# Optimization experiments

Hardware: AMD Instinct MI355X
Metric: run time of the kernel (lower is better)

The kernel has to match this reference:

```python
import jax, jax.numpy as jnp
import numpy as np

SEQ, BATCH, D_IN, D_HID, D_OUT = 2048, 256, 512, 512, 1000


def setup_inputs() -> dict:
    key = jax.random.key(0)
    ks = jax.random.split(key, 15)
    s_in = 1.0 / np.sqrt(D_IN)
    s_h = 1.0 / np.sqrt(D_HID)
    def lin(k, fan_in, shape, scale):
        return jax.random.uniform(k, shape, jnp.float32, -scale, scale)
    return {
        "x": jax.random.normal(ks[0], (SEQ, BATCH, D_IN), jnp.float32),
        # weights stored as [in, out] so y = x @ W + b
        "Wz": lin(ks[1], D_IN, (D_IN, D_HID), s_in),  "bz": lin(ks[2], D_IN, (D_HID,), s_in),
        "Uz": lin(ks[3], D_HID, (D_HID, D_HID), s_h), "buz": lin(ks[4], D_HID, (D_HID,), s_h),
        "Wr": lin(ks[5], D_IN, (D_IN, D_HID), s_in),  "br": lin(ks[6], D_IN, (D_HID,), s_in),
        "Ur": lin(ks[7], D_HID, (D_HID, D_HID), s_h), "bur": lin(ks[8], D_HID, (D_HID,), s_h),
        "Wh": lin(ks[9], D_IN, (D_IN, D_HID), s_in),  "bh": lin(ks[10], D_IN, (D_HID,), s_in),
        "Uh": lin(ks[11], D_HID, (D_HID, D_HID), s_h), "buh": lin(ks[12], D_HID, (D_HID,), s_h),
        "Wfc": lin(ks[13], D_HID, (D_HID, D_OUT), s_h), "bfc": lin(ks[14], D_HID, (D_OUT,), s_h),
    }


def reference(x, Wz, bz, Uz, buz, Wr, br, Ur, bur, Wh, bh, Uh, buh, Wfc, bfc):
    B, H = x.shape[1], Uz.shape[0]

    def gru_step(h, xt):
        # xt: [B, D_IN], h: [B, H]
        z = jax.nn.sigmoid(xt @ Wz + bz + h @ Uz + buz)
        r = jax.nn.sigmoid(xt @ Wr + br + h @ Ur + bur)
        h_tild = jnp.tanh(xt @ Wh + bh + (r * h) @ Uh + buh)
        h_new = (1.0 - z) * h + z * h_tild
        return h_new, None

    h0 = jnp.zeros((B, H), x.dtype)  # zero init hidden (broadcast-equivalent)
    h, _ = jax.lax.scan(gru_step, h0, x)
    out = jax.nn.relu(h) @ Wfc + bfc        # [B, D_OUT]
    out = out[None]                          # [1, B, D_OUT]
    return jax.nn.log_softmax(out, axis=1)  # dim=1 as in torch module
```

## Files before the change

### kernel.cpp

```cpp
#include <hip/hip_runtime.h>


typedef unsigned short ushort_t;
typedef unsigned int uint_t;
typedef __bf16 bf16_t;
typedef bf16_t bf16x8 __attribute__((ext_vector_type(8)));
typedef float f32x4 __attribute__((ext_vector_type(4)));
typedef uint_t u32x4 __attribute__((ext_vector_type(4)));

__device__ __forceinline__ ushort_t f2bf(float f) {
  uint_t u = __float_as_uint(f);
  u += 0x7FFFu + ((u >> 16) & 1u);
  return (ushort_t)(u >> 16);
}
__device__ __forceinline__ float bfu2f(uint_t h) { return __uint_as_float(h << 16); }

__device__ __forceinline__ uint_t atom_add_ret(uint_t* p, uint_t v) {
  uint_t old;
  asm volatile("global_atomic_add %0, %1, %2, off sc0\n\t"
               "s_waitcnt vmcnt(0)"
               : "=v"(old) : "v"(p), "v"(v) : "memory");
  return old;
}
__device__ __forceinline__ void atom_add_noret(uint_t* p, uint_t v) {
  asm volatile("global_atomic_add %0, %1, off" :: "v"(p), "v"(v) : "memory");
}

__global__ __launch_bounds__(256) void prep_kernel(
    const float* __restrict__ Wz, const float* __restrict__ Wr, const float* __restrict__ Wh,
    const float* __restrict__ Uz, const float* __restrict__ Ur, const float* __restrict__ Uh,
    const float* __restrict__ bz, const float* __restrict__ buz,
    const float* __restrict__ br, const float* __restrict__ bur,
    const float* __restrict__ bh, const float* __restrict__ buh,
    ushort_t* __restrict__ UT, ushort_t* __restrict__ WT, float* __restrict__ gbias)
{
  const int idx = blockIdx.x * 256 + threadIdx.x;
  {
    const int gate = idx >> 18, n = (idx >> 9) & 511, k = idx & 511;
    const float* U = (gate == 0) ? Uz : (gate == 1 ? Ur : Uh);
    UT[idx] = f2bf(U[k * 512 + n]);
  }
  {
    const int n = idx >> 9, k = idx & 511;
    const int gate = n >> 9, nn = n & 511;
    const float* W = (gate == 0) ? Wz : (gate == 1 ? Wr : Wh);
    WT[idx] = f2bf(W[k * 512 + nn]);
  }
  if (idx < 1536) {
    const int gate = idx >> 9, nn = idx & 511;
    gbias[idx] = (gate == 0) ? (bz[nn] + buz[nn])
               : (gate == 1) ? (br[nn] + bur[nn])
                             : (bh[nn] + buh[nn]);
  }
}

__global__ __launch_bounds__(256) void gate_gemm(
    const float* __restrict__ x,
    const ushort_t* __restrict__ WT,
    const float* __restrict__ gbias,
    ushort_t* __restrict__ gout,
    int mtiles)
{
  __shared__ ushort_t A_sh[128 * 72];
  __shared__ ushort_t B_sh[128 * 72];
  const int bid = blockIdx.x;
  int mt, nt;
  if ((mtiles & 31) == 0) {
    const int sb = bid / 384;
    const int r = bid - sb * 384;
    mt = sb * 32 + (r & 31);
    nt = r >> 5;
  } else {
    mt = bid / 12;
    nt = bid - mt * 12;
  }
  const int mrow0 = mt * 128;
  const int ncol0 = nt * 128;
  const int tid = threadIdx.x;
  const int wid = tid >> 6;
  const int lane = tid & 63;
  const int wm = wid >> 1, wn = wid & 1;
  const int l15 = lane & 15, l4 = lane >> 4;

  const f32x4 vzero = {0.f, 0.f, 0.f, 0.f};
  f32x4 acc[4][4];
#pragma unroll
  for (int m = 0; m < 4; ++m)
#pragma unroll
    for (int n = 0; n < 4; ++n) acc[m][n] = vzero;

  const int ar = tid >> 4, ak = tid & 15;
  const int bn = tid >> 3, bk = tid & 7;

  for (int ks = 0; ks < 8; ++ks) {
    if (ks) __syncthreads();
    const int k0 = ks * 64;
#pragma unroll
    for (int p = 0; p < 8; ++p) {
      const int r = p * 16 + ar;
      const float4 v = *(const float4*)&x[(size_t)(mrow0 + r) * 512 + (k0 + ak * 4)];
      ushort4 hv;
      hv.x = f2bf(v.x); hv.y = f2bf(v.y); hv.z = f2bf(v.z); hv.w = f2bf(v.w);
      *(ushort4*)&A_sh[r * 72 + ak * 4] = hv;
    }
#pragma unroll
    for (int p = 0; p < 4; ++p) {
      const int n = p * 32 + bn;
      *(uint4*)&B_sh[n * 72 + bk * 8] =
          *(const uint4*)&WT[(size_t)(ncol0 + n) * 512 + (k0 + bk * 8)];
    }
    __syncthreads();
#pragma unroll
    for (int kk = 0; kk < 2; ++kk) {
      bf16x8 a[4], b[4];
#pragma unroll
      for (int m = 0; m < 4; ++m)
        a[m] = *(const bf16x8*)&A_sh[(wm * 64 + m * 16 + l15) * 72 + kk * 32 + l4 * 8];
#pragma unroll
      for (int n = 0; n < 4; ++n)
        b[n] = *(const bf16x8*)&B_sh[(wn * 64 + n * 16 + l15) * 72 + kk * 32 + l4 * 8];
#pragma unroll
      for (int m = 0; m < 4; ++m)
#pragma unroll
        for (int n = 0; n < 4; ++n)
          acc[m][n] = __builtin_amdgcn_mfma_f32_16x16x32_bf16(a[m], b[n], acc[m][n], 0, 0, 0);
    }
  }
#pragma unroll
  for (int n = 0; n < 4; ++n) {
    const int gcol = ncol0 + wn * 64 + n * 16 + l15;
    const float bv = gbias[gcol];
#pragma unroll
    for (int m = 0; m < 4; ++m) {
      const int grow = mrow0 + wm * 64 + m * 16 + l4 * 4;
#pragma unroll
      for (int q = 0; q < 4; ++q)
        gout[(size_t)(grow + q) * 1536 + gcol] = f2bf(acc[m][n][q] + bv);
    }
  }
}

__device__ __forceinline__ bool group_barrier(uint_t* ctr, uint_t target, int tid, int* s_dead) {
  asm volatile("s_waitcnt vmcnt(0)" ::: "memory");
  __syncthreads();
  if (tid == 0) {
    atom_add_noret(ctr, 1u);
    int cnt = 0;
    for (;;) {
      const uint_t seen = atom_add_ret(ctr, 0u);
      if (seen >= target) break;
      __builtin_amdgcn_s_sleep(1);
      if (++cnt > (1 << 15)) { *s_dead = 1; break; }
    }
  }
  __syncthreads();
  return *s_dead != 0;
}

__device__ __forceinline__ void stage16x512(const ushort_t* __restrict__ src, int g, int j,
                                            ushort_t* dst_lds, int tid) {
  const ushort_t* p[4];
  int ridx[4];
#pragma unroll
  for (int k = 0; k < 4; ++k) {
    const int idx = (tid + (k << 8) + j * 64) & 1023;
    ridx[k] = idx;
    const int r = idx >> 6, kc = idx & 63;
    p[k] = src + (((g * 16 + r) << 9) + kc * 8);
  }
  u32x4 v0, v1, v2, v3;
  asm volatile(
      "global_load_dwordx4 %0, %4, off sc0\n\t"
      "global_load_dwordx4 %1, %5, off sc0\n\t"
      "global_load_dwordx4 %2, %6, off sc0\n\t"
      "global_load_dwordx4 %3, %7, off sc0\n\t"
      "s_waitcnt vmcnt(0)"
      : "=&v"(v0), "=&v"(v1), "=&v"(v2), "=&v"(v3)
      : "v"(p[0]), "v"(p[1]), "v"(p[2]), "v"(p[3])
      : "memory");
#pragma unroll
  for (int k = 0; k < 4; ++k) {
    const int r = ridx[k] >> 6, kc = ridx[k] & 63;
    *(u32x4*)&dst_lds[r * 520 + kc * 8] = (k == 0) ? v0 : (k == 1) ? v1 : (k == 2) ? v2 : v3;
  }
}

__global__ __launch_bounds__(256, 1) void gru_rec(
    const ushort_t* __restrict__ UT,
    const ushort_t* __restrict__ gates,
    ushort_t* __restrict__ h_buf,
    ushort_t* __restrict__ rh_buf,
    float* __restrict__ h_state,
    uint_t* __restrict__ bars,
    int Tc, int first)
{
  __shared__ ushort_t h_st[16 * 520];
  __shared__ float z_sh[512];
  __shared__ float hown[512];
  __shared__ float red[512];
  __shared__ int s_dead;

  const int tid = threadIdx.x;
  const int bid = blockIdx.x;
  const int g = bid & 15;
  const int j = bid >> 4;
  const int wid = tid >> 6;
  const int lane = tid & 63;
  const int l15 = lane & 15;
  const int l4 = lane >> 4;
  if (tid == 0) s_dead = 0;

  uint_t* ctr = bars + g * 64;
  uint_t nbar = 0;

  const int p1gate = wid >> 1;
  const int p1nt = wid & 1;
  const int p2nt = wid >> 1;
  const int p2kh = wid & 1;

  bf16x8 UB[16];
  {
    const size_t base = (size_t)((p1gate << 9) + j * 32 + p1nt * 16 + l15) * 512 + (size_t)(l4 * 8);
#pragma unroll
    for (int kk = 0; kk < 16; ++kk) UB[kk] = *(const bf16x8*)&UT[base + (size_t)kk * 32];
  }
  bf16x8 UH[8];
  {
    const size_t base = (size_t)(1024 + j * 32 + p2nt * 16 + l15) * 512 + (size_t)(p2kh * 256 + l4 * 8);
#pragma unroll
    for (int kk = 0; kk < 8; ++kk) UH[kk] = *(const bf16x8*)&UT[base + (size_t)kk * 32];
  }

  if (first) {
    for (int i = tid; i < 512; i += 256) {
      const int r = i >> 5, c = i & 31;
      h_buf[((g * 16 + r) << 9) + j * 32 + c] = 0;
      hown[i] = 0.f;
    }
  } else {
    for (int i = tid; i < 512; i += 256) {
      const int r = i >> 5, c = i & 31;
      hown[i] = h_state[((g * 16 + r) << 9) + j * 32 + c];
    }
  }
  if (group_barrier(ctr, (++nbar) * 16, tid, &s_dead)) return;

  const int colg1 = j * 32 + p1nt * 16 + l15;
  const int colg2 = j * 32 + p2nt * 16 + l15;

  uint_t c1u[4], c2u[4], n1u[4], n2u[4];
  {
    const size_t gb = (size_t)(g * 16) * 1536;
#pragma unroll
    for (int q = 0; q < 4; ++q) {
      n1u[q] = gates[gb + (size_t)(l4 * 4 + q) * 1536 + (p1gate << 9) + colg1];
      n2u[q] = gates[gb + (size_t)(l4 * 4 + q) * 1536 + 1024 + colg2];
    }
  }

  for (int tt = 0; tt < Tc; ++tt) {
    stage16x512(h_buf, g, j, h_st, tid);
    __syncthreads();
#pragma unroll
    for (int q = 0; q < 4; ++q) { c1u[q] = n1u[q]; c2u[q] = n2u[q]; }
    {
      const ushort_t* ap = &h_st[l15 * 520 + l4 * 8];
      f32x4 a0 = {0.f, 0.f, 0.f, 0.f}, a1 = {0.f, 0.f, 0.f, 0.f};
#pragma unroll
      for (int kk = 0; kk < 16; kk += 2) {
        a0 = __builtin_amdgcn_mfma_f32_16x16x32_bf16(*(const bf16x8*)(ap + kk * 32), UB[kk], a0, 0, 0, 0);
        a1 = __builtin_amdgcn_mfma_f32_16x16x32_bf16(*(const bf16x8*)(ap + kk * 32 + 32), UB[kk + 1], a1, 0, 0, 0);
      }
      const f32x4 acc = a0 + a1;
      const int lc = p1nt * 16 + l15;
#pragma unroll
      for (int q = 0; q < 4; ++q) {
        const int row = l4 * 4 + q;
        const float pre = acc[q] + bfu2f(c1u[q]);
        const float s = 1.f / (1.f + __expf(-pre));
        if (p1gate == 0) z_sh[row * 32 + lc] = s;
        else rh_buf[((g * 16 + row) << 9) + j * 32 + lc] = f2bf(s * hown[row * 32 + lc]);
      }
    }
    if (group_barrier(ctr, (++nbar) * 16, tid, &s_dead)) break;

    stage16x512(rh_buf, g, j, h_st, tid);
    __syncthreads();
    if (tt + 1 < Tc) {
      const size_t gb = (size_t)((size_t)(tt + 1) * 256 + g * 16) * 1536;
#pragma unroll
      for (int q = 0; q < 4; ++q) {
        n1u[q] = gates[gb + (size_t)(l4 * 4 + q) * 1536 + (p1gate << 9) + colg1];
        n2u[q] = gates[gb + (size_t)(l4 * 4 + q) * 1536 + 1024 + colg2];
      }
    }
    {
      const ushort_t* ap = &h_st[l15 * 520 + p2kh * 256 + l4 * 8];
      f32x4 a0 = {0.f, 0.f, 0.f, 0.f}, a1 = {0.f, 0.f, 0.f, 0.f};
#pragma unroll
      for (int kk = 0; kk < 8; kk += 2) {
        a0 = __builtin_amdgcn_mfma_f32_16x16x32_bf16(*(const bf16x8*)(ap + kk * 32), UH[kk], a0, 0, 0, 0);
        a1 = __builtin_amdgcn_mfma_f32_16x16x32_bf16(*(const bf16x8*)(ap + kk * 32 + 32), UH[kk + 1], a1, 0, 0, 0);
      }
      const f32x4 acc = a0 + a1;
      if (p2kh == 1) {
#pragma unroll
        for (int q = 0; q < 4; ++q) red[p2nt * 256 + (l4 * 4 + q) * 16 + l15] = acc[q];
      }
      __syncthreads();
      if (p2kh == 0) {
        const int lc = p2nt * 16 + l15;
#pragma unroll
        for (int q = 0; q < 4; ++q) {
          const int row = l4 * 4 + q;
          const float dot = acc[q] + red[p2nt * 256 + row * 16 + l15];
          float pre = dot + bfu2f(c2u[q]);
          pre = fminf(15.f, fmaxf(-15.f, pre));
          const float e = __expf(2.f * pre);
          const float th = (e - 1.f) / (e + 1.f);
          const float z = z_sh[row * 32 + lc];
          const float hold = hown[row * 32 + lc];
          const float hnew = (1.f - z) * hold + z * th;
          hown[row * 32 + lc] = hnew;
          h_buf[((g * 16 + row) << 9) + j * 32 + lc] = f2bf(hnew);
          if (tt == Tc - 1) h_state[((g * 16 + row) << 9) + j * 32 + lc] = hnew;
        }
      }
    }
    if (group_barrier(ctr, (++nbar) * 16, tid, &s_dead)) break;
  }
}

__global__ __launch_bounds__(256) void fc_kernel(
    const float* __restrict__ h, const float* __restrict__ Wfc,
    const float* __restrict__ bfc, float* __restrict__ logits)
{
  __shared__ float hsh[16][520];
  const int tid = threadIdx.x;
  const int by = blockIdx.y;
  {
    const int r = tid >> 4, seg = tid & 15;
    const float* src = &h[(size_t)(by * 16 + r) * 512 + seg * 32];
#pragma unroll
    for (int i = 0; i < 8; ++i) {
      float4 v = *(const float4*)&src[i * 4];
      v.x = fmaxf(v.x, 0.f); v.y = fmaxf(v.y, 0.f);
      v.z = fmaxf(v.z, 0.f); v.w = fmaxf(v.w, 0.f);
      *(float4*)&hsh[r][seg * 32 + i * 4] = v;
    }
  }
  __syncthreads();
  const int c = tid & 63, rq = tid >> 6;
  const int gc = blockIdx.x * 64 + c;
  if (gc >= 1000) return;
  float acc0 = 0.f, acc1 = 0.f, acc2 = 0.f, acc3 = 0.f;
  for (int k = 0; k < 512; ++k) {
    const float w = Wfc[(size_t)k * 1000 + gc];
    acc0 += hsh[rq * 4 + 0][k] * w;
    acc1 += hsh[rq * 4 + 1][k] * w;
    acc2 += hsh[rq * 4 + 2][k] * w;
    acc3 += hsh[rq * 4 + 3][k] * w;
  }
  const float bv = bfc[gc];
  const int r0 = by * 16 + rq * 4;
  logits[(size_t)(r0 + 0) * 1000 + gc] = acc0 + bv;
  logits[(size_t)(r0 + 1) * 1000 + gc] = acc1 + bv;
  logits[(size_t)(r0 + 2) * 1000 + gc] = acc2 + bv;
  logits[(size_t)(r0 + 3) * 1000 + gc] = acc3 + bv;
}

__global__ __launch_bounds__(256) void lsm_kernel(const float* __restrict__ logits,
                                                  float* __restrict__ out)
{
  const int c = blockIdx.x, tid = threadIdx.x;
  const int wid = tid >> 6, lane = tid & 63;
  __shared__ float red[8];
  const float v = logits[(size_t)tid * 1000 + c];
  float m = v;
#pragma unroll
  for (int o = 32; o >= 1; o >>= 1) m = fmaxf(m, __shfl_xor(m, o));
  if (lane == 0) red[wid] = m;
  __syncthreads();
  m = fmaxf(fmaxf(red[0], red[1]), fmaxf(red[2], red[3]));
  float s = __expf(v - m);
#pragma unroll
  for (int o = 32; o >= 1; o >>= 1) s += __shfl_xor(s, o);
  if (lane == 0) red[4 + wid] = s;
  __syncthreads();
  s = red[4] + red[5] + red[6] + red[7];
  out[(size_t)tid * 1000 + c] = (v - m) - __logf(s);
}

extern "C" void kernel_launch(void* const* d_in, const int* in_sizes, int n_in,
                              void* d_out, int out_size, void* d_ws, size_t ws_size,
                              hipStream_t stream) {
  (void)in_sizes; (void)n_in; (void)out_size;
  const float* x   = (const float*)d_in[0];
  const float* Wz  = (const float*)d_in[1];
  const float* bz  = (const float*)d_in[2];
  const float* Uz  = (const float*)d_in[3];
  const float* buz = (const float*)d_in[4];
  const float* Wr  = (const float*)d_in[5];
  const float* br  = (const float*)d_in[6];
  const float* Ur  = (const float*)d_in[7];
  const float* bur = (const float*)d_in[8];
  const float* Wh  = (const float*)d_in[9];
  const float* bh  = (const float*)d_in[10];
  const float* Uh  = (const float*)d_in[11];
  const float* buh = (const float*)d_in[12];
  const float* Wfc = (const float*)d_in[13];
  const float* bfc = (const float*)d_in[14];
  float* out = (float*)d_out;
  char* ws = (char*)d_ws;

  ushort_t* UT     = (ushort_t*)(ws + 0);
  ushort_t* WT     = (ushort_t*)(ws + 1572864);
  float*    gbias  = (float*)(ws + 3145728);
  ushort_t* h_buf  = (ushort_t*)(ws + 3151872);
  ushort_t* rh_buf = (ushort_t*)(ws + 3414016);
  float*    hstate = (float*)(ws + 3676160);
  float*    logits = (float*)(ws + 4200448);
  uint_t*   bars   = (uint_t*)(ws + 5224448);
  ushort_t* gates  = (ushort_t*)(ws + 5228544);

  const size_t fixed = 5228544;
  const size_t per_step = (size_t)256 * 1536 * 2;
  int Tc_max = 2048;
  if (ws_size < fixed + (size_t)2048 * per_step) {
    const size_t avail = (ws_size > fixed) ? (ws_size - fixed) : 0;
    Tc_max = (int)(avail / per_step);
    Tc_max &= ~15;
    if (Tc_max < 16) Tc_max = 16;
  }

  prep_kernel<<<3072, 256, 0, stream>>>(Wz, Wr, Wh, Uz, Ur, Uh,
                                        bz, buz, br, bur, bh, buh, UT, WT, gbias);

  int done = 0;
  while (done < 2048) {
    const int Tc = (2048 - done < Tc_max) ? (2048 - done) : Tc_max;
    const int mtiles = Tc * 2;
    gate_gemm<<<mtiles * 12, 256, 0, stream>>>(x + (size_t)done * 256 * 512, WT, gbias, gates, mtiles);
    hipMemsetAsync(bars, 0, 4096, stream);
    gru_rec<<<256, 256, 0, stream>>>(UT, gates, h_buf, rh_buf, hstate, bars, Tc, done == 0 ? 1 : 0);
    done += Tc;
  }
  fc_kernel<<<dim3(16, 16), 256, 0, stream>>>(hstate, Wfc, bfc, logits);
  lsm_kernel<<<1000, 256, 0, stream>>>(logits, out);
}
```

Baseline: 9.924 ms.

## Widen recurrent blocks to 1024 threads, cutting group barrier participants to four

The recurrent GRU kernel now launches 64 blocks of 1024 threads instead of 256 blocks of 256. Each block covers 128 hidden columns, so only 4 blocks per batch group meet at each cross-block barrier instead of 16. Each thread stages one 16-byte chunk instead of four. This aims to cut the global atomic barrier cost and the redundant staging of h per step, at the price of using fewer CUs and putting more registers and waves in each block.

```diff
diff --git a/kernel.cpp b/kernel.cpp
--- a/kernel.cpp
+++ b/kernel.cpp
@@ -159,33 +159,18 @@
 
 __device__ __forceinline__ void stage16x512(const ushort_t* __restrict__ src, int g, int j,
                                             ushort_t* dst_lds, int tid) {
-  const ushort_t* p[4];
-  int ridx[4];
-#pragma unroll
-  for (int k = 0; k < 4; ++k) {
-    const int idx = (tid + (k << 8) + j * 64) & 1023;
-    ridx[k] = idx;
-    const int r = idx >> 6, kc = idx & 63;
-    p[k] = src + (((g * 16 + r) << 9) + kc * 8);
-  }
-  u32x4 v0, v1, v2, v3;
+  const int idx = (tid + j * 256) & 1023;
+  const int r = idx >> 6, kc = idx & 63;
+  const ushort_t* p = src + (((g * 16 + r) << 9) + kc * 8);
+  u32x4 v0;
   asm volatile(
-      "global_load_dwordx4 %0, %4, off sc0\n\t"
-      "global_load_dwordx4 %1, %5, off sc0\n\t"
-      "global_load_dwordx4 %2, %6, off sc0\n\t"
-      "global_load_dwordx4 %3, %7, off sc0\n\t"
+      "global_load_dwordx4 %0, %1, off sc0\n\t"
       "s_waitcnt vmcnt(0)"
-      : "=&v"(v0), "=&v"(v1), "=&v"(v2), "=&v"(v3)
-      : "v"(p[0]), "v"(p[1]), "v"(p[2]), "v"(p[3])
-      : "memory");
-#pragma unroll
-  for (int k = 0; k < 4; ++k) {
-    const int r = ridx[k] >> 6, kc = ridx[k] & 63;
-    *(u32x4*)&dst_lds[r * 520 + kc * 8] = (k == 0) ? v0 : (k == 1) ? v1 : (k == 2) ? v2 : v3;
-  }
-}
-
-__global__ __launch_bounds__(256, 1) void gru_rec(
+      : "=&v"(v0) : "v"(p) : "memory");
+  *(u32x4*)&dst_lds[r * 520 + kc * 8] = v0;
+}
+
+__global__ __launch_bounds__(1024, 1) void gru_rec(
     const ushort_t* __restrict__ UT,
     const ushort_t* __restrict__ gates,
     ushort_t* __restrict__ h_buf,
@@ -195,9 +180,9 @@
     int Tc, int first)
 {
   __shared__ ushort_t h_st[16 * 520];
-  __shared__ float z_sh[512];
-  __shared__ float hown[512];
-  __shared__ float red[512];
+  __shared__ float z_sh[16 * 128];
+  __shared__ float hown[16 * 128];
+  __shared__ float red[8 * 256];
   __shared__ int s_dead;
 
   const int tid = threadIdx.x;
@@ -213,48 +198,48 @@
   uint_t* ctr = bars + g * 64;
   uint_t nbar = 0;
 
-  const int p1gate = wid >> 1;
-  const int p1nt = wid & 1;
+  const int p1gate = wid >> 3;
+  const int p1nt = wid & 7;
   const int p2nt = wid >> 1;
   const int p2kh = wid & 1;
 
   bf16x8 UB[16];
   {
-    const size_t base = (size_t)((p1gate << 9) + j * 32 + p1nt * 16 + l15) * 512 + (size_t)(l4 * 8);
+    const size_t base = (size_t)((p1gate << 9) + j * 128 + p1nt * 16 + l15) * 512 + (size_t)(l4 * 8);
 #pragma unroll
     for (int kk = 0; kk < 16; ++kk) UB[kk] = *(const bf16x8*)&UT[base + (size_t)kk * 32];
   }
   bf16x8 UH[8];
   {
-    const size_t base = (size_t)(1024 + j * 32 + p2nt * 16 + l15) * 512 + (size_t)(p2kh * 256 + l4 * 8);
+    const size_t base = (size_t)(1024 + j * 128 + p2nt * 16 + l15) * 512 + (size_t)(p2kh * 256 + l4 * 8);
 #pragma unroll
     for (int kk = 0; kk < 8; ++kk) UH[kk] = *(const bf16x8*)&UT[base + (size_t)kk * 32];
   }
 
   if (first) {
-    for (int i = tid; i < 512; i += 256) {
-      const int r = i >> 5, c = i & 31;
-      h_buf[((g * 16 + r) << 9) + j * 32 + c] = 0;
+    for (int i = tid; i < 2048; i += 1024) {
+      const int r = i >> 7, c = i & 127;
+      h_buf[((g * 16 + r) << 9) + j * 128 + c] = 0;
       hown[i] = 0.f;
     }
   } else {
-    for (int i = tid; i < 512; i += 256) {
-      const int r = i >> 5, c = i & 31;
-      hown[i] = h_state[((g * 16 + r) << 9) + j * 32 + c];
-    }
-  }
-  if (group_barrier(ctr, (++nbar) * 16, tid, &s_dead)) return;
-
-  const int colg1 = j * 32 + p1nt * 16 + l15;
-  const int colg2 = j * 32 + p2nt * 16 + l15;
+    for (int i = tid; i < 2048; i += 1024) {
+      const int r = i >> 7, c = i & 127;
+      hown[i] = h_state[((g * 16 + r) << 9) + j * 128 + c];
+    }
+  }
+  if (group_barrier(ctr, (++nbar) * 4, tid, &s_dead)) return;
+
+  const int colg1 = (p1gate << 9) + j * 128 + p1nt * 16 + l15;
+  const int colg2 = 1024 + j * 128 + p2nt * 16 + l15;
 
   uint_t c1u[4], c2u[4], n1u[4], n2u[4];
   {
     const size_t gb = (size_t)(g * 16) * 1536;
 #pragma unroll
     for (int q = 0; q < 4; ++q) {
-      n1u[q] = gates[gb + (size_t)(l4 * 4 + q) * 1536 + (p1gate << 9) + colg1];
-      n2u[q] = gates[gb + (size_t)(l4 * 4 + q) * 1536 + 1024 + colg2];
+      n1u[q] = gates[gb + (size_t)(l4 * 4 + q) * 1536 + colg1];
+      n2u[q] = gates[gb + (size_t)(l4 * 4 + q) * 1536 + colg2];
     }
   }
 
@@ -278,11 +263,11 @@
         const int row = l4 * 4 + q;
         const float pre = acc[q] + bfu2f(c1u[q]);
         const float s = 1.f / (1.f + __expf(-pre));
-        if (p1gate == 0) z_sh[row * 32 + lc] = s;
-        else rh_buf[((g * 16 + row) << 9) + j * 32 + lc] = f2bf(s * hown[row * 32 + lc]);
-      }
-    }
-    if (group_barrier(ctr, (++nbar) * 16, tid, &s_dead)) break;
+        if (p1gate == 0) z_sh[row * 128 + lc] = s;
+        else rh_buf[((g * 16 + row) << 9) + j * 128 + lc] = f2bf(s * hown[row * 128 + lc]);
+      }
+    }
+    if (group_barrier(ctr, (++nbar) * 4, tid, &s_dead)) break;
 
     stage16x512(rh_buf, g, j, h_st, tid);
     __syncthreads();
@@ -290,8 +275,8 @@
       const size_t gb = (size_t)((size_t)(tt + 1) * 256 + g * 16) * 1536;
 #pragma unroll
       for (int q = 0; q < 4; ++q) {
-        n1u[q] = gates[gb + (size_t)(l4 * 4 + q) * 1536 + (p1gate << 9) + colg1];
-        n2u[q] = gates[gb + (size_t)(l4 * 4 + q) * 1536 + 1024 + colg2];
+        n1u[q] = gates[gb + (size_t)(l4 * 4 + q) * 1536 + colg1];
+        n2u[q] = gates[gb + (size_t)(l4 * 4 + q) * 1536 + colg2];
       }
     }
     {
@@ -318,16 +303,16 @@
           pre = fminf(15.f, fmaxf(-15.f, pre));
           const float e = __expf(2.f * pre);
           const float th = (e - 1.f) / (e + 1.f);
-          const float z = z_sh[row * 32 + lc];
-          const float hold = hown[row * 32 + lc];
+          const float z = z_sh[row * 128 + lc];
+          const float hold = hown[row * 128 + lc];
           const float hnew = (1.f - z) * hold + z * th;
-          hown[row * 32 + lc] = hnew;
-          h_buf[((g * 16 + row) << 9) + j * 32 + lc] = f2bf(hnew);
-          if (tt == Tc - 1) h_state[((g * 16 + row) << 9) + j * 32 + lc] = hnew;
+          hown[row * 128 + lc] = hnew;
+          h_buf[((g * 16 + row) << 9) + j * 128 + lc] = f2bf(hnew);
+          if (tt == Tc - 1) h_state[((g * 16 + row) << 9) + j * 128 + lc] = hnew;
         }
       }
     }
-    if (group_barrier(ctr, (++nbar) * 16, tid, &s_dead)) break;
+    if (group_barrier(ctr, (++nbar) * 4, tid, &s_dead)) break;
   }
 }
 
@@ -442,7 +427,7 @@
     const int mtiles = Tc * 2;
     gate_gemm<<<mtiles * 12, 256, 0, stream>>>(x + (size_t)done * 256 * 512, WT, gbias, gates, mtiles);
     hipMemsetAsync(bars, 0, 4096, stream);
-    gru_rec<<<256, 256, 0, stream>>>(UT, gates, h_buf, rh_buf, hstate, bars, Tc, done == 0 ? 1 : 0);
+    gru_rec<<<64, 1024, 0, stream>>>(UT, gates, h_buf, rh_buf, hstate, bars, Tc, done == 0 ? 1 : 0);
     done += Tc;
   }
   fc_kernel<<<dim3(16, 16), 256, 0, stream>>>(hstate, Wfc, bfc, logits);
```

Result: slower. 22.24 ms (+124.1%).

## Fuse input-gate GEMM into persistent recurrent kernel with extra producer waves

Applied to the files above, without the earlier changes.

Removes the separate gate_gemm kernel and its large global gates buffer. The recurrent kernel now launches 512 threads per block. Four extra waves keep their slice of W in registers and compute the x·W gate projections two timesteps ahead into a triple-buffered LDS ring. They also prefetch and convert the next x slice while the recurrent waves run, hiding the input GEMM inside the barrier-bound recurrence and avoiding the write and reread of the gates tensor. The cost is doubled block size, higher register and LDS pressure, and extra work on the sequential critical path between barriers.

```diff
diff --git a/kernel.cpp b/kernel.cpp
--- a/kernel.cpp
+++ b/kernel.cpp
@@ -54,92 +54,6 @@
   }
 }
 
-__global__ __launch_bounds__(256) void gate_gemm(
-    const float* __restrict__ x,
-    const ushort_t* __restrict__ WT,
-    const float* __restrict__ gbias,
-    ushort_t* __restrict__ gout,
-    int mtiles)
-{
-  __shared__ ushort_t A_sh[128 * 72];
-  __shared__ ushort_t B_sh[128 * 72];
-  const int bid = blockIdx.x;
-  int mt, nt;
-  if ((mtiles & 31) == 0) {
-    const int sb = bid / 384;
-    const int r = bid - sb * 384;
-    mt = sb * 32 + (r & 31);
-    nt = r >> 5;
-  } else {
-    mt = bid / 12;
-    nt = bid - mt * 12;
-  }
-  const int mrow0 = mt * 128;
-  const int ncol0 = nt * 128;
-  const int tid = threadIdx.x;
-  const int wid = tid >> 6;
-  const int lane = tid & 63;
-  const int wm = wid >> 1, wn = wid & 1;
-  const int l15 = lane & 15, l4 = lane >> 4;
-
-  const f32x4 vzero = {0.f, 0.f, 0.f, 0.f};
-  f32x4 acc[4][4];
-#pragma unroll
-  for (int m = 0; m < 4; ++m)
-#pragma unroll
-    for (int n = 0; n < 4; ++n) acc[m][n] = vzero;
-
-  const int ar = tid >> 4, ak = tid & 15;
-  const int bn = tid >> 3, bk = tid & 7;
-
-  for (int ks = 0; ks < 8; ++ks) {
-    if (ks) __syncthreads();
-    const int k0 = ks * 64;
-#pragma unroll
-    for (int p = 0; p < 8; ++p) {
-      const int r = p * 16 + ar;
-      const float4 v = *(const float4*)&x[(size_t)(mrow0 + r) * 512 + (k0 + ak * 4)];
-      ushort4 hv;
-      hv.x = f2bf(v.x); hv.y = f2bf(v.y); hv.z = f2bf(v.z); hv.w = f2bf(v.w);
-      *(ushort4*)&A_sh[r * 72 + ak * 4] = hv;
-    }
-#pragma unroll
-    for (int p = 0; p < 4; ++p) {
-      const int n = p * 32 + bn;
-      *(uint4*)&B_sh[n * 72 + bk * 8] =
-          *(const uint4*)&WT[(size_t)(ncol0 + n) * 512 + (k0 + bk * 8)];
-    }
-    __syncthreads();
-#pragma unroll
-    for (int kk = 0; kk < 2; ++kk) {
-      bf16x8 a[4], b[4];
-#pragma unroll
-      for (int m = 0; m < 4; ++m)
-        a[m] = *(const bf16x8*)&A_sh[(wm * 64 + m * 16 + l15) * 72 + kk * 32 + l4 * 8];
-#pragma unroll
-      for (int n = 0; n < 4; ++n)
-        b[n] = *(const bf16x8*)&B_sh[(wn * 64 + n * 16 + l15) * 72 + kk * 32 + l4 * 8];
-#pragma unroll
-      for (int m = 0; m < 4; ++m)
-#pragma unroll
-        for (int n = 0; n < 4; ++n)
-          acc[m][n] = __builtin_amdgcn_mfma_f32_16x16x32_bf16(a[m], b[n], acc[m][n], 0, 0, 0);
-    }
-  }
-#pragma unroll
-  for (int n = 0; n < 4; ++n) {
-    const int gcol = ncol0 + wn * 64 + n * 16 + l15;
-    const float bv = gbias[gcol];
-#pragma unroll
-    for (int m = 0; m < 4; ++m) {
-      const int grow = mrow0 + wm * 64 + m * 16 + l4 * 4;
-#pragma unroll
-      for (int q = 0; q < 4; ++q)
-        gout[(size_t)(grow + q) * 1536 + gcol] = f2bf(acc[m][n][q] + bv);
-    }
-  }
-}
-
 __device__ __forceinline__ bool group_barrier(uint_t* ctr, uint_t target, int tid, int* s_dead) {
   asm volatile("s_waitcnt vmcnt(0)" ::: "memory");
   __syncthreads();
@@ -185,16 +99,34 @@
   }
 }
 
-__global__ __launch_bounds__(256, 1) void gru_rec(
+__device__ __forceinline__ void stage_x_direct(const float* __restrict__ src_base,
+                                               ushort_t* dst, int tid2) {
+  const int row = tid2 >> 4, seg = tid2 & 15;
+  const float* src = src_base + (size_t)row * 512 + seg * 32;
+  ushort_t* d = dst + row * 520 + seg * 32;
+#pragma unroll
+  for (int i = 0; i < 8; ++i) {
+    const float4 v = ((const float4*)src)[i];
+    ushort4 hv;
+    hv.x = f2bf(v.x); hv.y = f2bf(v.y); hv.z = f2bf(v.z); hv.w = f2bf(v.w);
+    ((ushort4*)d)[i] = hv;
+  }
+}
+
+__global__ __launch_bounds__(512, 1) void gru_rec(
     const ushort_t* __restrict__ UT,
-    const ushort_t* __restrict__ gates,
+    const ushort_t* __restrict__ WT,
+    const float* __restrict__ gbias,
+    const float* __restrict__ x,
     ushort_t* __restrict__ h_buf,
     ushort_t* __restrict__ rh_buf,
     float* __restrict__ h_state,
     uint_t* __restrict__ bars,
-    int Tc, int first)
+    int first)
 {
   __shared__ ushort_t h_st[16 * 520];
+  __shared__ ushort_t x_lds[16 * 520];
+  __shared__ ushort_t gates_lds[3 * 16 * 96];
   __shared__ float z_sh[512];
   __shared__ float hown[512];
   __shared__ float red[512];
@@ -213,57 +145,92 @@
   uint_t* ctr = bars + g * 64;
   uint_t nbar = 0;
 
-  const int p1gate = wid >> 1;
+  const bool isrec = (wid < 4);
+  const int p1gate = (wid >> 1) & 1;
   const int p1nt = wid & 1;
-  const int p2nt = wid >> 1;
+  const int p2nt = (wid >> 1) & 1;
   const int p2kh = wid & 1;
-
-  bf16x8 UB[16];
-  {
-    const size_t base = (size_t)((p1gate << 9) + j * 32 + p1nt * 16 + l15) * 512 + (size_t)(l4 * 8);
-#pragma unroll
-    for (int kk = 0; kk < 16; ++kk) UB[kk] = *(const bf16x8*)&UT[base + (size_t)kk * 32];
-  }
-  bf16x8 UH[8];
-  {
-    const size_t base = (size_t)(1024 + j * 32 + p2nt * 16 + l15) * 512 + (size_t)(p2kh * 256 + l4 * 8);
-#pragma unroll
-    for (int kk = 0; kk < 8; ++kk) UH[kk] = *(const bf16x8*)&UT[base + (size_t)kk * 32];
-  }
-
-  if (first) {
-    for (int i = tid; i < 512; i += 256) {
-      const int r = i >> 5, c = i & 31;
-      h_buf[((g * 16 + r) << 9) + j * 32 + c] = 0;
-      hown[i] = 0.f;
-    }
-  } else {
-    for (int i = tid; i < 512; i += 256) {
-      const int r = i >> 5, c = i & 31;
-      hown[i] = h_state[((g * 16 + r) << 9) + j * 32 + c];
+  const int gw = wid - 4;
+  const int gatesel = (gw < 2) ? gw : 2;
+  const int t0 = (gw < 2) ? 0 : (gw - 2);
+  const int ntile = (gw < 2) ? 2 : 1;
+  const int tid2 = tid & 255;
+  const int xrow = tid2 >> 4, xseg = tid2 & 15;
+
+  bf16x8 UB[16], UH[8];
+  if (isrec) {
+    const size_t b1 = (size_t)((p1gate << 9) + j * 32 + p1nt * 16 + l15) * 512 + (size_t)(l4 * 8);
+#pragma unroll
+    for (int kk = 0; kk < 16; ++kk) UB[kk] = *(const bf16x8*)&UT[b1 + (size_t)kk * 32];
+    const size_t b2 = (size_t)(1024 + j * 32 + p2nt * 16 + l15) * 512 + (size_t)(p2kh * 256 + l4 * 8);
+#pragma unroll
+    for (int kk = 0; kk < 8; ++kk) UH[kk] = *(const bf16x8*)&UT[b2 + (size_t)kk * 32];
+  }
+  bf16x8 WF[32];
+  float gb0 = 0.f, gb1 = 0.f;
+  if (!isrec) {
+#pragma unroll
+    for (int s = 0; s < 2; ++s) {
+      if (s < ntile) {
+        const size_t wb = (size_t)(gatesel * 512 + j * 32 + (t0 + s) * 16 + l15) * 512 + (size_t)(l4 * 8);
+#pragma unroll
+        for (int kk = 0; kk < 16; ++kk) WF[s * 16 + kk] = *(const bf16x8*)&WT[wb + (size_t)kk * 32];
+      }
+    }
+    gb0 = gbias[gatesel * 512 + j * 32 + t0 * 16 + l15];
+    if (ntile == 2) gb1 = gbias[gatesel * 512 + j * 32 + 16 + l15];
+  }
+
+  if (isrec) {
+    if (first) {
+      for (int i = tid; i < 512; i += 256) {
+        const int r = i >> 5, c = i & 31;
+        h_buf[((g * 16 + r) << 9) + j * 32 + c] = 0;
+        hown[i] = 0.f;
+      }
+    } else {
+      for (int i = tid; i < 512; i += 256) {
+        const int r = i >> 5, c = i & 31;
+        hown[i] = h_state[((g * 16 + r) << 9) + j * 32 + c];
+      }
     }
   }
   if (group_barrier(ctr, (++nbar) * 16, tid, &s_dead)) return;
 
-  const int colg1 = j * 32 + p1nt * 16 + l15;
-  const int colg2 = j * 32 + p2nt * 16 + l15;
-
-  uint_t c1u[4], c2u[4], n1u[4], n2u[4];
-  {
-    const size_t gb = (size_t)(g * 16) * 1536;
-#pragma unroll
-    for (int q = 0; q < 4; ++q) {
-      n1u[q] = gates[gb + (size_t)(l4 * 4 + q) * 1536 + (p1gate << 9) + colg1];
-      n2u[q] = gates[gb + (size_t)(l4 * 4 + q) * 1536 + 1024 + colg2];
-    }
-  }
-
-  for (int tt = 0; tt < Tc; ++tt) {
-    stage16x512(h_buf, g, j, h_st, tid);
+  for (int w = 0; w < 2; ++w) {
+    if (!isrec) stage_x_direct(x + ((size_t)w * 256 + g * 16) * 512, x_lds, tid2);
     __syncthreads();
-#pragma unroll
-    for (int q = 0; q < 4; ++q) { c1u[q] = n1u[q]; c2u[q] = n2u[q]; }
-    {
+    if (!isrec) {
+      f32x4 ac0 = {0.f, 0.f, 0.f, 0.f}, ac1 = {0.f, 0.f, 0.f, 0.f};
+#pragma unroll
+      for (int kk = 0; kk < 16; ++kk) {
+        const bf16x8 xa = *(const bf16x8*)&x_lds[l15 * 520 + kk * 32 + l4 * 8];
+        ac0 = __builtin_amdgcn_mfma_f32_16x16x32_bf16(xa, WF[kk], ac0, 0, 0, 0);
+        if (ntile == 2)
+          ac1 = __builtin_amdgcn_mfma_f32_16x16x32_bf16(xa, WF[16 + kk], ac1, 0, 0, 0);
+      }
+#pragma unroll
+      for (int q = 0; q < 4; ++q) {
+        const int row = l4 * 4 + q;
+        gates_lds[w * 1536 + row * 96 + gatesel * 32 + t0 * 16 + l15] = f2bf(ac0[q] + gb0);
+        if (ntile == 2)
+          gates_lds[w * 1536 + row * 96 + gatesel * 32 + 16 + l15] = f2bf(ac1[q] + gb1);
+      }
+    }
+    __syncthreads();
+  }
+  if (!isrec) stage_x_direct(x + ((size_t)2 * 256 + g * 16) * 512, x_lds, tid2);
+  __syncthreads();
+
+  for (int tt = 0; tt < 2048; ++tt) {
+    const int slot_r = tt % 3;
+    const int slot_w = (tt + 2) % 3;
+    const bool do_gemm = (tt + 2 < 2048);
+    const bool do_x = (tt + 3 < 2048);
+
+    if (isrec) stage16x512(h_buf, g, j, h_st, tid);
+    __syncthreads();
+    if (isrec) {
       const ushort_t* ap = &h_st[l15 * 520 + l4 * 8];
       f32x4 a0 = {0.f, 0.f, 0.f, 0.f}, a1 = {0.f, 0.f, 0.f, 0.f};
 #pragma unroll
@@ -276,25 +243,39 @@
 #pragma unroll
       for (int q = 0; q < 4; ++q) {
         const int row = l4 * 4 + q;
-        const float pre = acc[q] + bfu2f(c1u[q]);
+        const float pre = acc[q] + bfu2f(gates_lds[slot_r * 1536 + row * 96 + p1gate * 32 + lc]);
         const float s = 1.f / (1.f + __expf(-pre));
         if (p1gate == 0) z_sh[row * 32 + lc] = s;
         else rh_buf[((g * 16 + row) << 9) + j * 32 + lc] = f2bf(s * hown[row * 32 + lc]);
       }
+    } else if (do_gemm && gw < 2) {
+      f32x4 ac0 = {0.f, 0.f, 0.f, 0.f}, ac1 = {0.f, 0.f, 0.f, 0.f};
+#pragma unroll
+      for (int kk = 0; kk < 16; ++kk) {
+        const bf16x8 xa = *(const bf16x8*)&x_lds[l15 * 520 + kk * 32 + l4 * 8];
+        ac0 = __builtin_amdgcn_mfma_f32_16x16x32_bf16(xa, WF[kk], ac0, 0, 0, 0);
+        ac1 = __builtin_amdgcn_mfma_f32_16x16x32_bf16(xa, WF[16 + kk], ac1, 0, 0, 0);
+      }
+#pragma unroll
+      for (int q = 0; q < 4; ++q) {
+        const int row = l4 * 4 + q;
+        gates_lds[slot_w * 1536 + row * 96 + gatesel * 32 + l15] = f2bf(ac0[q] + gb0);
+        gates_lds[slot_w * 1536 + row * 96 + gatesel * 32 + 16 + l15] = f2bf(ac1[q] + gb1);
+      }
     }
     if (group_barrier(ctr, (++nbar) * 16, tid, &s_dead)) break;
 
-    stage16x512(rh_buf, g, j, h_st, tid);
+    float4 xr[8];
+    if (isrec) {
+      stage16x512(rh_buf, g, j, h_st, tid);
+    } else if (do_x) {
+      const float* src = x + ((size_t)(tt + 3) * 256 + g * 16) * 512 + (size_t)xrow * 512 + xseg * 32;
+#pragma unroll
+      for (int i = 0; i < 8; ++i) xr[i] = ((const float4*)src)[i];
+    }
     __syncthreads();
-    if (tt + 1 < Tc) {
-      const size_t gb = (size_t)((size_t)(tt + 1) * 256 + g * 16) * 1536;
-#pragma unroll
-      for (int q = 0; q < 4; ++q) {
-        n1u[q] = gates[gb + (size_t)(l4 * 4 + q) * 1536 + (p1gate << 9) + colg1];
-        n2u[q] = gates[gb + (size_t)(l4 * 4 + q) * 1536 + 1024 + colg2];
-      }
-    }
-    {
+    f32x4 acc2 = {0.f, 0.f, 0.f, 0.f};
+    if (isrec) {
       const ushort_t* ap = &h_st[l15 * 520 + p2kh * 256 + l4 * 8];
       f32x4 a0 = {0.f, 0.f, 0.f, 0.f}, a1 = {0.f, 0.f, 0.f, 0.f};
 #pragma unroll
@@ -302,19 +283,33 @@
         a0 = __builtin_amdgcn_mfma_f32_16x16x32_bf16(*(const bf16x8*)(ap + kk * 32), UH[kk], a0, 0, 0, 0);
         a1 = __builtin_amdgcn_mfma_f32_16x16x32_bf16(*(const bf16x8*)(ap + kk * 32 + 32), UH[kk + 1], a1, 0, 0, 0);
       }
-      const f32x4 acc = a0 + a1;
+      acc2 = a0 + a1;
       if (p2kh == 1) {
 #pragma unroll
-        for (int q = 0; q < 4; ++q) red[p2nt * 256 + (l4 * 4 + q) * 16 + l15] = acc[q];
-      }
-      __syncthreads();
+        for (int q = 0; q < 4; ++q) red[p2nt * 256 + (l4 * 4 + q) * 16 + l15] = acc2[q];
+      }
+    } else if (do_gemm && gw >= 2) {
+      f32x4 ac0 = {0.f, 0.f, 0.f, 0.f};
+#pragma unroll
+      for (int kk = 0; kk < 16; ++kk) {
+        const bf16x8 xa = *(const bf16x8*)&x_lds[l15 * 520 + kk * 32 + l4 * 8];
+        ac0 = __builtin_amdgcn_mfma_f32_16x16x32_bf16(xa, WF[kk], ac0, 0, 0, 0);
+      }
+#pragma unroll
+      for (int q = 0; q < 4; ++q) {
+        const int row = l4 * 4 + q;
+        gates_lds[slot_w * 1536 + row * 96 + 64 + t0 * 16 + l15] = f2bf(ac0[q] + gb0);
+      }
+    }
+    __syncthreads();
+    if (isrec) {
       if (p2kh == 0) {
         const int lc = p2nt * 16 + l15;
 #pragma unroll
         for (int q = 0; q < 4; ++q) {
           const int row = l4 * 4 + q;
-          const float dot = acc[q] + red[p2nt * 256 + row * 16 + l15];
-          float pre = dot + bfu2f(c2u[q]);
+          const float dot = acc2[q] + red[p2nt * 256 + row * 16 + l15];
+          float pre = dot + bfu2f(gates_lds[slot_r * 1536 + row * 96 + 64 + lc]);
           pre = fminf(15.f, fmaxf(-15.f, pre));
           const float e = __expf(2.f * pre);
           const float th = (e - 1.f) / (e + 1.f);
@@ -323,8 +318,16 @@
           const float hnew = (1.f - z) * hold + z * th;
           hown[row * 32 + lc] = hnew;
           h_buf[((g * 16 + row) << 9) + j * 32 + lc] = f2bf(hnew);
-          if (tt == Tc - 1) h_state[((g * 16 + row) << 9) + j * 32 + lc] = hnew;
+          if (tt == 2047) h_state[((g * 16 + row) << 9) + j * 32 + lc] = hnew;
         }
+      }
+    } else if (do_x) {
+      ushort_t* d = x_lds + xrow * 520 + xseg * 32;
+#pragma unroll
+      for (int i = 0; i < 8; ++i) {
+        ushort4 hv;
+        hv.x = f2bf(xr[i].x); hv.y = f2bf(xr[i].y); hv.z = f2bf(xr[i].z); hv.w = f2bf(xr[i].w);
+        ((ushort4*)d)[i] = hv;
       }
     }
     if (group_barrier(ctr, (++nbar) * 16, tid, &s_dead)) break;
@@ -394,7 +397,7 @@
 extern "C" void kernel_launch(void* const* d_in, const int* in_sizes, int n_in,
                               void* d_out, int out_size, void* d_ws, size_t ws_size,
                               hipStream_t stream) {
-  (void)in_sizes; (void)n_in; (void)out_size;
+  (void)in_sizes; (void)n_in; (void)out_size; (void)ws_size;
   const float* x   = (const float*)d_in[0];
   const float* Wz  = (const float*)d_in[1];
   const float* bz  = (const float*)d_in[2];
@@ -421,30 +424,11 @@
   float*    hstate = (float*)(ws + 3676160);
   float*    logits = (float*)(ws + 4200448);
   uint_t*   bars   = (uint_t*)(ws + 5224448);
-  ushort_t* gates  = (ushort_t*)(ws + 5228544);
-
-  const size_t fixed = 5228544;
-  const size_t per_step = (size_t)256 * 1536 * 2;
-  int Tc_max = 2048;
-  if (ws_size < fixed + (size_t)2048 * per_step) {
-    const size_t avail = (ws_size > fixed) ? (ws_size - fixed) : 0;
-    Tc_max = (int)(avail / per_step);
-    Tc_max &= ~15;
-    if (Tc_max < 16) Tc_max = 16;
-  }
 
   prep_kernel<<<3072, 256, 0, stream>>>(Wz, Wr, Wh, Uz, Ur, Uh,
                                         bz, buz, br, bur, bh, buh, UT, WT, gbias);
-
-  int done = 0;
-  while (done < 2048) {
-    const int Tc = (2048 - done < Tc_max) ? (2048 - done) : Tc_max;
-    const int mtiles = Tc * 2;
-    gate_gemm<<<mtiles * 12, 256, 0, stream>>>(x + (size_t)done * 256 * 512, WT, gbias, gates, mtiles);
-    hipMemsetAsync(bars, 0, 4096, stream);
-    gru_rec<<<256, 256, 0, stream>>>(UT, gates, h_buf, rh_buf, hstate, bars, Tc, done == 0 ? 1 : 0);
-    done += Tc;
-  }
+  hipMemsetAsync(bars, 0, 4096, stream);
+  gru_rec<<<256, 512, 0, stream>>>(UT, WT, gbias, x, h_buf, rh_buf, hstate, bars, 1);
   fc_kernel<<<dim3(16, 16), 256, 0, stream>>>(hstate, Wfc, bfc, logits);
   lsm_kernel<<<1000, 256, 0, stream>>>(logits, out);
 }
```

Result: slower. 15.21 ms (+53.3%).
